# Optimization experiments

Measured on AMD Instinct MI355X. Metric: run time of the kernel, lower is better.

Reference implementation:

```python
import jax, jax.numpy as jnp
import numpy as np

B, L, S, H, E = 4, 1024, 1024, 16, 64
TOP_K = 10


def setup_inputs() -> dict:
    key = jax.random.key(0)
    kq, kk, kv = jax.random.split(key, 3)
    queries = jax.random.normal(kq, (B, L, H, E), dtype=jnp.float32)
    keys = jax.random.normal(kk, (B, S, H, E), dtype=jnp.float32)
    values = jax.random.normal(kv, (B, S, H, E), dtype=jnp.float32)
    return {"queries": queries, "keys": keys, "values": values}


def reference(queries, keys, values):
    Bq, Lq, Hq, Eq = queries.shape
    Sq = keys.shape[1]
    scale = 1.0 / np.sqrt(Eq).astype(np.float32)

    # FFT-based top-k frequency selection (mirrors torch: rfft over seq dim, ortho norm)
    keys_flat = keys.transpose(0, 2, 1, 3).reshape(Bq * Hq, Sq, Eq)  # [BH, S, E]
    freqs = jnp.fft.rfft(keys_flat, axis=1, norm='ortho')            # [BH, S//2+1, E]
    freq_mags = jnp.abs(freqs).mean(axis=-1)                          # [BH, S//2+1]
    k = min(TOP_K, Sq, freq_mags.shape[1])
    _, top_idx = jax.lax.top_k(freq_mags, k)                          # [BH, k]

    # Vectorized scatter of top-k indices into boolean position mask [BH, S]
    sparse_mask = jnp.zeros((Bq * Hq, Sq), dtype=bool)
    sparse_mask = sparse_mask.at[jnp.arange(Bq * Hq)[:, None], top_idx].set(True)
    sparse_mask = sparse_mask.reshape(Bq, Hq, Sq)                     # [B, H, S]

    # Dense masked attention
    scores = jnp.einsum('blhe,bshe->bhls', queries, keys) * scale     # [B, H, L, S]
    scores = jnp.where(sparse_mask[:, :, None, :], scores, -jnp.inf)
    attn = jax.nn.softmax(scores, axis=-1)                            # dropout: eval mode (identity)
    out = jnp.einsum('bhls,bshe->blhe', attn, values)                 # [B, L, H, E]
    return out, attn
```

## Files before the change

### kernel.cpp

```cpp
#include <hip/hip_runtime.h>
#include <math.h>

#define Bc 4
#define Lc 1024
#define Sc 1024
#define Hc 16
#define Ec 64
#define BHc 64
#define NF 513
#define TOPK 10
#define ECH 8
#define NCH 8

__global__ __launch_bounds__(512) void fft_chunk_kernel(
    const float* __restrict__ keys, float* __restrict__ pmag) {
  __shared__ float2 data[ECH][1025];
  __shared__ float2 tw[512];

  const int t   = threadIdx.x;
  const int blk = blockIdx.x;
  const int bh  = blk & 63;
  const int ch  = blk >> 6;
  const int b   = bh >> 4, h = bh & 15;
  const int e0  = ch * ECH;

  {
    float ang = -6.28318530717958647692f * (float)t / 1024.0f;
    float sn, cs;
    sincosf(ang, &sn, &cs);
    tw[t] = make_float2(cs, sn);
  }

  for (int i = t; i < ECH * 1024; i += 512) {
    int e = i & (ECH - 1);
    int s = i >> 3;
    float v = keys[(((size_t)b * Sc + s) * Hc + h) * Ec + e0 + e];
    int rs = __brev((unsigned)s) >> 22;
    data[e][rs] = make_float2(v, 0.0f);
  }
  __syncthreads();

  for (int st = 0; st < 10; ++st) {
    const int half = 1 << st;
    const int j  = t & (half - 1);
    const int i0 = ((t >> st) << (st + 1)) + j;
    const int i1 = i0 + half;
    const float2 W = tw[j << (9 - st)];
#pragma unroll
    for (int col = 0; col < ECH; ++col) {
      float2 u = data[col][i0];
      float2 v = data[col][i1];
      float vr = v.x * W.x - v.y * W.y;
      float vi = v.x * W.y + v.y * W.x;
      data[col][i0] = make_float2(u.x + vr, u.y + vi);
      data[col][i1] = make_float2(u.x - vr, u.y - vi);
    }
    __syncthreads();
  }

  for (int f = t; f < NF; f += 512) {
    float ssum = 0.0f;
#pragma unroll
    for (int c = 0; c < ECH; ++c) {
      float2 z = data[c][f];
      ssum += sqrtf(z.x * z.x + z.y * z.y);
    }
    pmag[(size_t)blk * NF + f] = ssum;
  }
}

__global__ __launch_bounds__(256) void topk_kernel(
    const float* __restrict__ pmag, int* __restrict__ idx_out) {
  __shared__ float mag[NF];
  __shared__ float redv[4];
  __shared__ int   redi[4];
  __shared__ int   topi[TOPK];

  const int bh = blockIdx.x;
  const int t  = threadIdx.x;

  for (int f = t; f < NF; f += 256) {
    float s = 0.0f;
#pragma unroll
    for (int ch = 0; ch < NCH; ++ch)
      s += pmag[(size_t)(ch * 64 + bh) * NF + f];
    mag[f] = s;
  }
  __syncthreads();

  for (int r = 0; r < TOPK; ++r) {
    float bv = -INFINITY;
    int   bi = 0x7fffffff;
    for (int f = t; f < NF; f += 256) {
      float v = mag[f];
      if (v > bv || (v == bv && f < bi)) { bv = v; bi = f; }
    }
#pragma unroll
    for (int off = 32; off > 0; off >>= 1) {
      float ov = __shfl_xor(bv, off);
      int   oi = __shfl_xor(bi, off);
      if (ov > bv || (ov == bv && oi < bi)) { bv = ov; bi = oi; }
    }
    if ((t & 63) == 0) { redv[t >> 6] = bv; redi[t >> 6] = bi; }
    __syncthreads();
    if (t == 0) {
      for (int w = 1; w < 4; ++w)
        if (redv[w] > bv || (redv[w] == bv && redi[w] < bi)) {
          bv = redv[w]; bi = redi[w];
        }
      topi[r] = bi;
      mag[bi] = -INFINITY;
    }
    __syncthreads();
  }
  if (t < TOPK) idx_out[bh * 16 + t] = topi[t];
}

__global__ __launch_bounds__(256) void attn_kernel(
    const float* __restrict__ qs, const float* __restrict__ ks,
    const float* __restrict__ vs, const int* __restrict__ idx,
    float* __restrict__ out, float* __restrict__ attn) {
  __shared__ float prow[4][1024];

  const int bh   = blockIdx.x;
  const int b    = bh >> 4, h = bh & 15;
  const int l0   = blockIdx.y * 64;
  const int lane = threadIdx.x & 63;
  const int wave = threadIdx.x >> 6;

  for (int i = threadIdx.x; i < 4 * 1024; i += 256)
    (&prow[0][0])[i] = 0.0f;

  int id[TOPK];
  float kreg[TOPK], vreg[TOPK];
#pragma unroll
  for (int j = 0; j < TOPK; ++j) {
    id[j] = idx[bh * 16 + j];
    size_t base = (((size_t)b * Sc + id[j]) * Hc + h) * Ec + lane;
    kreg[j] = ks[base];
    vreg[j] = vs[base];
  }
  int myid = 0;
#pragma unroll
  for (int j = 0; j < TOPK; ++j) myid = (lane == j) ? id[j] : myid;
  __syncthreads();

  for (int li = 0; li < 16; ++li) {
    const int l = l0 + wave * 16 + li;
    float q = qs[(((size_t)b * Lc + l) * Hc + h) * Ec + lane];

    float p[TOPK];
#pragma unroll
    for (int j = 0; j < TOPK; ++j) p[j] = q * kreg[j];
#pragma unroll
    for (int j = 0; j < TOPK; ++j) {
      float v = p[j];
#pragma unroll
      for (int off = 32; off > 0; off >>= 1) v += __shfl_xor(v, off);
      p[j] = v * 0.125f;
    }
    float mx = p[0];
#pragma unroll
    for (int j = 1; j < TOPK; ++j) mx = fmaxf(mx, p[j]);
    float ssum = 0.0f;
#pragma unroll
    for (int j = 0; j < TOPK; ++j) { p[j] = __expf(p[j] - mx); ssum += p[j]; }
    float inv = 1.0f / ssum;
    float o = 0.0f;
#pragma unroll
    for (int j = 0; j < TOPK; ++j) { p[j] *= inv; o = fmaf(p[j], vreg[j], o); }

    out[(((size_t)b * Lc + l) * Hc + h) * Ec + lane] = o;

    float myp = 0.0f;
#pragma unroll
    for (int j = 0; j < TOPK; ++j) myp = (lane == j) ? p[j] : myp;
    if (lane < TOPK) prow[wave][myid] = myp;

    float* arow = attn + ((size_t)bh * Lc + l) * Sc;
#pragma unroll
    for (int i = 0; i < 4; ++i) {
      float4 vv = ((const float4*)&prow[wave][0])[lane + 64 * i];
      ((float4*)arow)[lane + 64 * i] = vv;
    }
    if (lane < TOPK) prow[wave][myid] = 0.0f;
  }
}

extern "C" void kernel_launch(void* const* d_in, const int* in_sizes, int n_in,
                              void* d_out, int out_size, void* d_ws,
                              size_t ws_size, hipStream_t stream) {
  (void)in_sizes; (void)n_in; (void)out_size; (void)ws_size;
  const float* qs = (const float*)d_in[0];
  const float* ks = (const float*)d_in[1];
  const float* vs = (const float*)d_in[2];

  float* out  = (float*)d_out;
  float* attn = out + (size_t)Bc * Lc * Hc * Ec;

  float* pmag = (float*)d_ws;
  int*   idxs = (int*)((char*)d_ws +
                       (size_t)(NCH * BHc) * NF * sizeof(float));

  fft_chunk_kernel<<<NCH * BHc, 512, 0, stream>>>(ks, pmag);
  topk_kernel<<<BHc, 256, 0, stream>>>(pmag, idxs);
  attn_kernel<<<dim3(BHc, 16), 256, 0, stream>>>(qs, ks, vs, idxs, out, attn);
}
```

Before: 373.3 us.

## Use radix-4 FFT with real-pair packing, single-wave top-k, and tiled attention

```diff
diff --git a/kernel.cpp b/kernel.cpp
--- a/kernel.cpp
+++ b/kernel.cpp
@@ -9,77 +9,103 @@
 #define BHc 64
 #define NF 513
 #define TOPK 10
-#define ECH 8
 #define NCH 8
-
-__global__ __launch_bounds__(512) void fft_chunk_kernel(
+#define COLW 2304
+
+#define PADW(w) ((w) + (((w) >> 4) << 1))
+#define ZADDR(col, i) ((col) * COLW + PADW(2 * (i)))
+
+__global__ __launch_bounds__(512) void fft4_kernel(
     const float* __restrict__ keys, float* __restrict__ pmag) {
-  __shared__ float2 data[ECH][1025];
-  __shared__ float2 tw[512];
+  __shared__ float zbuf[4 * COLW];
+  __shared__ float2 tw[1024];
 
   const int t   = threadIdx.x;
   const int blk = blockIdx.x;
   const int bh  = blk & 63;
   const int ch  = blk >> 6;
   const int b   = bh >> 4, h = bh & 15;
-  const int e0  = ch * ECH;
-
-  {
-    float ang = -6.28318530717958647692f * (float)t / 1024.0f;
+
+  for (int m = t; m < 1024; m += 512) {
     float sn, cs;
-    sincosf(ang, &sn, &cs);
-    tw[t] = make_float2(cs, sn);
-  }
-
-  for (int i = t; i < ECH * 1024; i += 512) {
-    int e = i & (ECH - 1);
-    int s = i >> 3;
-    float v = keys[(((size_t)b * Sc + s) * Hc + h) * Ec + e0 + e];
-    int rs = __brev((unsigned)s) >> 22;
-    data[e][rs] = make_float2(v, 0.0f);
-  }
-  __syncthreads();
-
-  for (int st = 0; st < 10; ++st) {
-    const int half = 1 << st;
-    const int j  = t & (half - 1);
-    const int i0 = ((t >> st) << (st + 1)) + j;
-    const int i1 = i0 + half;
-    const float2 W = tw[j << (9 - st)];
-#pragma unroll
-    for (int col = 0; col < ECH; ++col) {
-      float2 u = data[col][i0];
-      float2 v = data[col][i1];
-      float vr = v.x * W.x - v.y * W.y;
-      float vi = v.x * W.y + v.y * W.x;
-      data[col][i0] = make_float2(u.x + vr, u.y + vi);
-      data[col][i1] = make_float2(u.x - vr, u.y - vi);
+    sincosf(-6.28318530717958647692f * (float)m * (1.0f / 1024.0f), &sn, &cs);
+    tw[m] = make_float2(cs, sn);
+  }
+
+  const float4* k4 = (const float4*)keys;
+  const int fbase = b * 262144 + h * 16 + ch * 2;
+  for (int i = t; i < 2048; i += 512) {
+    const int s  = i >> 1;
+    const int q4 = i & 1;
+    float4 v = k4[fbase + s * 256 + q4];
+    unsigned r = __brev((unsigned)s) >> 22;
+    unsigned rs = ((r & 0x2AAu) >> 1) | ((r & 0x155u) << 1);
+    *(float2*)&zbuf[ZADDR(2 * q4, rs)]     = make_float2(v.x, v.y);
+    *(float2*)&zbuf[ZADDR(2 * q4 + 1, rs)] = make_float2(v.z, v.w);
+  }
+  __syncthreads();
+
+  for (int st = 0; st < 5; ++st) {
+    const int quarter = 1 << (2 * st);
+    const int tstep   = 256 >> (2 * st);
+#pragma unroll
+    for (int rep = 0; rep < 2; ++rep) {
+      const int task = t + rep * 512;
+      const int col  = task >> 8;
+      const int bf   = task & 255;
+      const int j    = bf & (quarter - 1);
+      const int bas  = ((bf >> (2 * st)) << (2 * st + 2)) + j;
+
+      const float2 w1 = tw[j * tstep];
+      const float2 w2 = tw[2 * j * tstep];
+      const float2 w3 = tw[3 * j * tstep];
+
+      float2 a  = *(const float2*)&zbuf[ZADDR(col, bas)];
+      float2 bb = *(const float2*)&zbuf[ZADDR(col, bas + quarter)];
+      float2 c  = *(const float2*)&zbuf[ZADDR(col, bas + 2 * quarter)];
+      float2 d  = *(const float2*)&zbuf[ZADDR(col, bas + 3 * quarter)];
+
+      float2 bw = make_float2(bb.x * w1.x - bb.y * w1.y, bb.x * w1.y + bb.y * w1.x);
+      float2 cw = make_float2(c.x * w2.x - c.y * w2.y, c.x * w2.y + c.y * w2.x);
+      float2 dw = make_float2(d.x * w3.x - d.y * w3.y, d.x * w3.y + d.y * w3.x);
+
+      float2 s0 = make_float2(a.x + cw.x, a.y + cw.y);
+      float2 s1 = make_float2(a.x - cw.x, a.y - cw.y);
+      float2 s2 = make_float2(bw.x + dw.x, bw.y + dw.y);
+      float2 s3 = make_float2(bw.x - dw.x, bw.y - dw.y);
+
+      *(float2*)&zbuf[ZADDR(col, bas)]               = make_float2(s0.x + s2.x, s0.y + s2.y);
+      *(float2*)&zbuf[ZADDR(col, bas + quarter)]     = make_float2(s1.x + s3.y, s1.y - s3.x);
+      *(float2*)&zbuf[ZADDR(col, bas + 2 * quarter)] = make_float2(s0.x - s2.x, s0.y - s2.y);
+      *(float2*)&zbuf[ZADDR(col, bas + 3 * quarter)] = make_float2(s1.x - s3.y, s1.y + s3.x);
     }
     __syncthreads();
   }
 
   for (int f = t; f < NF; f += 512) {
+    const int nf = (1024 - f) & 1023;
     float ssum = 0.0f;
 #pragma unroll
-    for (int c = 0; c < ECH; ++c) {
-      float2 z = data[c][f];
-      ssum += sqrtf(z.x * z.x + z.y * z.y);
+    for (int c = 0; c < 4; ++c) {
+      float2 zf = *(const float2*)&zbuf[ZADDR(c, f)];
+      float2 zn = *(const float2*)&zbuf[ZADDR(c, nf)];
+      float xr = 0.5f * (zf.x + zn.x);
+      float xi = 0.5f * (zf.y - zn.y);
+      float yr = 0.5f * (zf.y + zn.y);
+      float yi = 0.5f * (zn.x - zf.x);
+      ssum += sqrtf(xr * xr + xi * xi) + sqrtf(yr * yr + yi * yi);
     }
     pmag[(size_t)blk * NF + f] = ssum;
   }
 }
 
-__global__ __launch_bounds__(256) void topk_kernel(
+__global__ __launch_bounds__(64) void topk_kernel(
     const float* __restrict__ pmag, int* __restrict__ idx_out) {
   __shared__ float mag[NF];
-  __shared__ float redv[4];
-  __shared__ int   redi[4];
-  __shared__ int   topi[TOPK];
-
   const int bh = blockIdx.x;
   const int t  = threadIdx.x;
 
-  for (int f = t; f < NF; f += 256) {
+  for (int f = t; f < NF; f += 64) {
     float s = 0.0f;
 #pragma unroll
     for (int ch = 0; ch < NCH; ++ch)
@@ -91,7 +117,7 @@
   for (int r = 0; r < TOPK; ++r) {
     float bv = -INFINITY;
     int   bi = 0x7fffffff;
-    for (int f = t; f < NF; f += 256) {
+    for (int f = t; f < NF; f += 64) {
       float v = mag[f];
       if (v > bv || (v == bv && f < bi)) { bv = v; bi = f; }
     }
@@ -101,89 +127,102 @@
       int   oi = __shfl_xor(bi, off);
       if (ov > bv || (ov == bv && oi < bi)) { bv = ov; bi = oi; }
     }
-    if ((t & 63) == 0) { redv[t >> 6] = bv; redi[t >> 6] = bi; }
+    if (t == 0) {
+      idx_out[bh * 16 + r] = bi;
+      mag[bi] = -INFINITY;
+    }
     __syncthreads();
-    if (t == 0) {
-      for (int w = 1; w < 4; ++w)
-        if (redv[w] > bv || (redv[w] == bv && redi[w] < bi)) {
-          bv = redv[w]; bi = redi[w];
-        }
-      topi[r] = bi;
-      mag[bi] = -INFINITY;
-    }
-    __syncthreads();
-  }
-  if (t < TOPK) idx_out[bh * 16 + t] = topi[t];
+  }
 }
 
 __global__ __launch_bounds__(256) void attn_kernel(
     const float* __restrict__ qs, const float* __restrict__ ks,
     const float* __restrict__ vs, const int* __restrict__ idx,
     float* __restrict__ out, float* __restrict__ attn) {
+  __shared__ float qt[64][65];
+  __shared__ float kvt[2][TOPK][64];
+  __shared__ float sc[64][13];
+  __shared__ int   sid[TOPK];
   __shared__ float prow[4][1024];
 
+  const int t    = threadIdx.x;
   const int bh   = blockIdx.x;
   const int b    = bh >> 4, h = bh & 15;
   const int l0   = blockIdx.y * 64;
-  const int lane = threadIdx.x & 63;
-  const int wave = threadIdx.x >> 6;
-
-  for (int i = threadIdx.x; i < 4 * 1024; i += 256)
-    (&prow[0][0])[i] = 0.0f;
-
-  int id[TOPK];
-  float kreg[TOPK], vreg[TOPK];
-#pragma unroll
-  for (int j = 0; j < TOPK; ++j) {
-    id[j] = idx[bh * 16 + j];
-    size_t base = (((size_t)b * Sc + id[j]) * Hc + h) * Ec + lane;
-    kreg[j] = ks[base];
-    vreg[j] = vs[base];
-  }
-  int myid = 0;
-#pragma unroll
-  for (int j = 0; j < TOPK; ++j) myid = (lane == j) ? id[j] : myid;
+  const int wave = t >> 6;
+  const int lane = t & 63;
+
+  if (t < TOPK) sid[t] = idx[bh * 16 + t];
+  for (int i = t; i < 4 * 1024; i += 256) (&prow[0][0])[i & 4095] = 0.0f;
+
+  {
+    const float4* q4 = (const float4*)qs;
+    const int fb = b * 262144 + h * 16;
+    for (int i = t; i < 1024; i += 256) {
+      const int row = i >> 4, c4 = i & 15;
+      float4 v = q4[fb + (l0 + row) * 256 + c4];
+      qt[row][c4 * 4 + 0] = v.x;
+      qt[row][c4 * 4 + 1] = v.y;
+      qt[row][c4 * 4 + 2] = v.z;
+      qt[row][c4 * 4 + 3] = v.w;
+    }
+  }
+  __syncthreads();
+
+  for (int i = t; i < 2 * TOPK * 64; i += 256) {
+    const int kv = i >= TOPK * 64;
+    const int j  = (i >> 6) - kv * TOPK;
+    const int e  = i & 63;
+    const float* src = kv ? vs : ks;
+    kvt[kv][j][e] = src[(size_t)b * 1048576 + (size_t)sid[j] * 1024 + h * 64 + e];
+  }
+  __syncthreads();
+
+#pragma unroll
+  for (int r = 0; r < 3; ++r) {
+    const int task = r * 256 + t;
+    const int j = task >> 6;
+    const int l = task & 63;
+    if (j < TOPK) {
+      float acc = 0.0f;
+#pragma unroll 8
+      for (int e = 0; e < 64; ++e) acc += qt[l][e] * kvt[0][j][e];
+      sc[l][j] = acc * 0.125f;
+    }
+  }
+  __syncthreads();
+
+  if (t < 64) {
+    float pv[TOPK];
+    float mx = -INFINITY;
+#pragma unroll
+    for (int j = 0; j < TOPK; ++j) { pv[j] = sc[t][j]; mx = fmaxf(mx, pv[j]); }
+    float sum = 0.0f;
+#pragma unroll
+    for (int j = 0; j < TOPK; ++j) { pv[j] = __expf(pv[j] - mx); sum += pv[j]; }
+    float inv = 1.0f / sum;
+#pragma unroll
+    for (int j = 0; j < TOPK; ++j) sc[t][j] = pv[j] * inv;
+  }
   __syncthreads();
 
   for (int li = 0; li < 16; ++li) {
-    const int l = l0 + wave * 16 + li;
-    float q = qs[(((size_t)b * Lc + l) * Hc + h) * Ec + lane];
-
-    float p[TOPK];
-#pragma unroll
-    for (int j = 0; j < TOPK; ++j) p[j] = q * kreg[j];
-#pragma unroll
-    for (int j = 0; j < TOPK; ++j) {
-      float v = p[j];
-#pragma unroll
-      for (int off = 32; off > 0; off >>= 1) v += __shfl_xor(v, off);
-      p[j] = v * 0.125f;
-    }
-    float mx = p[0];
-#pragma unroll
-    for (int j = 1; j < TOPK; ++j) mx = fmaxf(mx, p[j]);
-    float ssum = 0.0f;
-#pragma unroll
-    for (int j = 0; j < TOPK; ++j) { p[j] = __expf(p[j] - mx); ssum += p[j]; }
-    float inv = 1.0f / ssum;
+    const int l = wave * 16 + li;
+
     float o = 0.0f;
 #pragma unroll
-    for (int j = 0; j < TOPK; ++j) { p[j] *= inv; o = fmaf(p[j], vreg[j], o); }
-
-    out[(((size_t)b * Lc + l) * Hc + h) * Ec + lane] = o;
-
-    float myp = 0.0f;
-#pragma unroll
-    for (int j = 0; j < TOPK; ++j) myp = (lane == j) ? p[j] : myp;
-    if (lane < TOPK) prow[wave][myid] = myp;
-
-    float* arow = attn + ((size_t)bh * Lc + l) * Sc;
+    for (int j = 0; j < TOPK; ++j) o += sc[l][j] * kvt[1][j][lane];
+    out[((size_t)b * 1024 + l0 + l) * 1024 + h * 64 + lane] = o;
+
+    if (lane < TOPK) prow[wave][sid[lane]] = sc[l][lane];
+
+    float* arow = attn + ((size_t)bh * 1024 + l0 + l) * 1024;
 #pragma unroll
     for (int i = 0; i < 4; ++i) {
-      float4 vv = ((const float4*)&prow[wave][0])[lane + 64 * i];
-      ((float4*)arow)[lane + 64 * i] = vv;
-    }
-    if (lane < TOPK) prow[wave][myid] = 0.0f;
+      float4 vv = *(const float4*)&prow[wave][4 * lane + 256 * i];
+      *(float4*)&arow[4 * lane + 256 * i] = vv;
+    }
+    if (lane < TOPK) prow[wave][sid[lane]] = 0.0f;
   }
 }
 
@@ -199,10 +238,9 @@
   float* attn = out + (size_t)Bc * Lc * Hc * Ec;
 
   float* pmag = (float*)d_ws;
-  int*   idxs = (int*)((char*)d_ws +
-                       (size_t)(NCH * BHc) * NF * sizeof(float));
-
-  fft_chunk_kernel<<<NCH * BHc, 512, 0, stream>>>(ks, pmag);
-  topk_kernel<<<BHc, 256, 0, stream>>>(pmag, idxs);
+  int*   idxs = (int*)((char*)d_ws + (size_t)(NCH * BHc) * NF * sizeof(float));
+
+  fft4_kernel<<<NCH * BHc, 512, 0, stream>>>(ks, pmag);
+  topk_kernel<<<BHc, 64, 0, stream>>>(pmag, idxs);
   attn_kernel<<<dim3(BHc, 16), 256, 0, stream>>>(qs, ks, vs, idxs, out, attn);
 }
```

New measurement: 355.9 us. 1.05x faster.
